# Optimization experiments

Measured on AMD Instinct MI355X. Metric: run time of the kernel, lower is better.

The kernel has to match this reference:

```python
import jax, jax.numpy as jnp
import numpy as np

D_MODEL = 768
N_HEADS = 12
D_K = D_MODEL // N_HEADS


def setup_inputs() -> dict:
    key = jax.random.key(0)
    ks = jax.random.split(key, 9)
    B, S = 4, 2048
    sc = 1.0 / np.sqrt(D_MODEL)
    inp = {"x": jax.random.normal(ks[0], (B, S, D_MODEL), dtype=jnp.float32)}
    names = ["q", "k", "v", "o"]
    for i, n in enumerate(names):
        inp[f"W{n}"] = jax.random.normal(ks[1 + 2 * i], (D_MODEL, D_MODEL), dtype=jnp.float32) * sc
        inp[f"b{n}"] = jax.random.normal(ks[2 + 2 * i], (D_MODEL,), dtype=jnp.float32) * 0.01
    return inp


def reference(x, Wq, bq, Wk, bk, Wv, bv, Wo, bo):
    B, S, _ = x.shape
    def split_heads(t):  # [B,S,D] -> [B,H,S,d_k]
        return t.reshape(B, S, N_HEADS, D_K).transpose(0, 2, 1, 3)
    Q = split_heads(x @ Wq.T + bq)
    K = split_heads(x @ Wk.T + bk)
    V = split_heads(x @ Wv.T + bv)
    # NOTE: original divides by d_k, not sqrt(d_k)
    scores = jnp.einsum("bhqd,bhkd->bhqk", Q, K) / D_K
    scores = jax.nn.softmax(scores, axis=-1)
    att = jnp.einsum("bhqk,bhkd->bhqd", scores, V)  # [B,H,S,d_k]
    att = att.transpose(0, 2, 1, 3).reshape(B, S, D_MODEL)
    return att @ Wo.T + bo
```

## Files before the change

### kernel.cpp

```cpp
#include <hip/hip_runtime.h>
#include <hip/hip_bf16.h>

typedef __bf16 bf16;
typedef _Float16 f16;
typedef bf16 bf16x8 __attribute__((ext_vector_type(8)));
typedef bf16 bf16x4 __attribute__((ext_vector_type(4)));
typedef f16 f16x4 __attribute__((ext_vector_type(4)));
typedef float f32x4 __attribute__((ext_vector_type(4)));

#define SLEN 2048
#define HEADS 12
#define DMODEL 768

#define GLOAD16(g, l) \
    __builtin_amdgcn_global_load_lds((const __attribute__((address_space(1))) void*)(g), \
                                     (__attribute__((address_space(3))) void*)(l), 16, 0, 0)

__global__ void cvt_kernel(const float* __restrict__ src, bf16* __restrict__ dst, int n4) {
    int idx = blockIdx.x * blockDim.x + threadIdx.x;
    if (idx < n4) {
        float4 v = ((const float4*)src)[idx];
        bf16x4 o;
        o[0] = (bf16)v.x; o[1] = (bf16)v.y; o[2] = (bf16)v.z; o[3] = (bf16)v.w;
        *(bf16x4*)(dst + (size_t)idx * 4) = o;
    }
}

__global__ void cvt4_kernel(const float* __restrict__ s0, const float* __restrict__ s1,
                            const float* __restrict__ s2, const float* __restrict__ s3,
                            bf16* __restrict__ d0, bf16* __restrict__ d1,
                            bf16* __restrict__ d2, bf16* __restrict__ d3, int n4) {
    const float* s; bf16* d;
    switch (blockIdx.y) {
        case 0: s = s0; d = d0; break;
        case 1: s = s1; d = d1; break;
        case 2: s = s2; d = d2; break;
        default: s = s3; d = d3; break;
    }
    int idx = blockIdx.x * blockDim.x + threadIdx.x;
    if (idx < n4) {
        float4 v = ((const float4*)s)[idx];
        bf16x4 o;
        o[0] = (bf16)v.x; o[1] = (bf16)v.y; o[2] = (bf16)v.z; o[3] = (bf16)v.w;
        *(bf16x4*)(d + (size_t)idx * 4) = o;
    }
}

__global__ __launch_bounds__(256, 3) void gemm_qkv(
    const bf16* __restrict__ A, const bf16* __restrict__ Bw,
    const float* __restrict__ bq, const float* __restrict__ bk, const float* __restrict__ bv,
    bf16* __restrict__ Qb, bf16* __restrict__ Kb, f16* __restrict__ VTb)
{
    __shared__ __align__(16) char smem[34048];
    typedef bf16 Tile[128][32];
    Tile* As = (Tile*)smem;
    Tile* Bs = (Tile*)(smem + 16384);
    const int K = DMODEL;
    int tid = threadIdx.x;
    int w = tid >> 6, lane = tid & 63, i16 = lane & 15, q4 = lane >> 4;
    int mblk = (w & 1) * 64, nblk = (w >> 1) * 64;
    int row0 = blockIdx.y * 128, col0 = blockIdx.x * 128;
    int srow = (lane >> 2), scol = (lane & 3) * 8;
    f32x4 acc[4][4] = {};

    const bf16* Ab = A  + (size_t)(row0 + w * 16 + srow) * K + scol;
    const bf16* Bb = Bw + (size_t)(col0 + w * 16 + srow) * K + scol;

#define STAGE(buf, k0) do { \
        GLOAD16(Ab + (k0),                  &As[buf][w * 16][0]); \
        GLOAD16(Ab + (size_t)64 * K + (k0), &As[buf][w * 16 + 64][0]); \
        GLOAD16(Bb + (k0),                  &Bs[buf][w * 16][0]); \
        GLOAD16(Bb + (size_t)64 * K + (k0), &Bs[buf][w * 16 + 64][0]); \
    } while (0)

    STAGE(0, 0);
    __syncthreads();
    int buf = 0;
    for (int k0 = 0; k0 < K; k0 += 32, buf ^= 1) {
        if (k0 + 32 < K) STAGE(buf ^ 1, k0 + 32);
        bf16x8 af[4], bfr[4];
#pragma unroll
        for (int t = 0; t < 4; ++t) af[t] = *(const bf16x8*)(&As[buf][mblk + t * 16 + i16][q4 * 8]);
#pragma unroll
        for (int t = 0; t < 4; ++t) bfr[t] = *(const bf16x8*)(&Bs[buf][nblk + t * 16 + i16][q4 * 8]);
#pragma unroll
        for (int ct = 0; ct < 4; ++ct)
#pragma unroll
            for (int st = 0; st < 4; ++st)
                acc[ct][st] = __builtin_amdgcn_mfma_f32_16x16x32_bf16(bfr[ct], af[st], acc[ct][st], 0, 0, 0);
        __syncthreads();
    }
#undef STAGE

    int region = col0 / DMODEL;
    int cbase = col0 - region * DMODEL + nblk;

    if (region < 2) {
        const float* bias = region ? bk : bq;
        bf16* dstb = region ? Kb : Qb;
        float scale = region ? 1.0f : 0.0225421217f;
#pragma unroll
        for (int ct = 0; ct < 4; ++ct) {
#pragma unroll
            for (int st = 0; st < 4; ++st) {
                int c0 = cbase + ct * 16 + q4 * 4;
                int h = c0 >> 6, d0 = c0 & 63;
                int sg = row0 + mblk + st * 16 + i16;
                int b = sg >> 11, s = sg & 2047;
                float4 bb = *(const float4*)(bias + c0);
                bf16x4 o;
                if (region == 0) {
                    o[0] = (bf16)((acc[ct][st][0] + bb.x) * scale);
                    o[1] = (bf16)((acc[ct][st][1] + bb.y) * scale);
                    o[2] = (bf16)((acc[ct][st][2] + bb.z) * scale);
                    o[3] = (bf16)((acc[ct][st][3] + bb.w) * scale);
                } else {
                    o[0] = (bf16)(acc[ct][st][0] + bb.x);
                    o[1] = (bf16)(acc[ct][st][1] + bb.y);
                    o[2] = (bf16)(acc[ct][st][2] + bb.z);
                    o[3] = (bf16)(acc[ct][st][3] + bb.w);
                }
                *(bf16x4*)(dstb + (((size_t)(b * HEADS + h)) * SLEN + s) * 64 + d0) = o;
            }
        }
    } else {
        __syncthreads();
        f16 (*Cs)[132] = (f16(*)[132])smem;
#pragma unroll
        for (int ct = 0; ct < 4; ++ct) {
#pragma unroll
            for (int st = 0; st < 4; ++st) {
                int cg = cbase + ct * 16 + q4 * 4;
                float4 bb = *(const float4*)(bv + cg);
                f16x4 vv;
                vv[0] = (f16)(acc[ct][st][0] + bb.x);
                vv[1] = (f16)(acc[ct][st][1] + bb.y);
                vv[2] = (f16)(acc[ct][st][2] + bb.z);
                vv[3] = (f16)(acc[ct][st][3] + bb.w);
                *(f16x4*)(&Cs[mblk + st * 16 + i16][nblk + ct * 16 + q4 * 4]) = vv;
            }
        }
        __syncthreads();
        int cl = lane * 2;
        int cg = cbase - nblk + cl;
        int h = cg >> 6, d = cg & 63;
        int s0 = w * 32;
        int b = row0 >> 11, sg = (row0 & 2047) + s0;
        f16* dst0 = VTb + ((size_t)(b * HEADS + h) * 64 + d) * SLEN + sg;
        f16* dst1 = dst0 + SLEN;
#pragma unroll
        for (int j = 0; j < 4; ++j) {
            unsigned v[8];
#pragma unroll
            for (int i = 0; i < 8; ++i) v[i] = *(const unsigned*)(&Cs[s0 + j * 8 + i][cl]);
            unsigned lo[4], hi[4];
#pragma unroll
            for (int i = 0; i < 4; ++i) {
                lo[i] = (v[2 * i] & 0xffffu) | (v[2 * i + 1] << 16);
                hi[i] = (v[2 * i] >> 16) | (v[2 * i + 1] & 0xffff0000u);
            }
            *(uint4*)(dst0 + j * 8) = *(uint4*)lo;
            *(uint4*)(dst1 + j * 8) = *(uint4*)hi;
        }
    }
}

__global__ __launch_bounds__(256, 3) void gemm_out(
    const bf16* __restrict__ A, const bf16* __restrict__ Bw,
    const float* __restrict__ bo, float* __restrict__ out)
{
    __shared__ bf16 As[2][128][32];
    __shared__ bf16 Bs[2][128][32];
    const int K = DMODEL;
    int tid = threadIdx.x;
    int w = tid >> 6, lane = tid & 63, i16 = lane & 15, q4 = lane >> 4;
    int mblk = (w & 1) * 64, nblk = (w >> 1) * 64;
    int row0 = blockIdx.y * 128, col0 = blockIdx.x * 128;
    int srow = (lane >> 2), scol = (lane & 3) * 8;
    f32x4 acc[4][4] = {};

    const bf16* Ab = A  + (size_t)(row0 + w * 16 + srow) * K + scol;
    const bf16* Bb = Bw + (size_t)(col0 + w * 16 + srow) * K + scol;

#define STAGE(buf, k0) do { \
        GLOAD16(Ab + (k0),                  &As[buf][w * 16][0]); \
        GLOAD16(Ab + (size_t)64 * K + (k0), &As[buf][w * 16 + 64][0]); \
        GLOAD16(Bb + (k0),                  &Bs[buf][w * 16][0]); \
        GLOAD16(Bb + (size_t)64 * K + (k0), &Bs[buf][w * 16 + 64][0]); \
    } while (0)

    STAGE(0, 0);
    __syncthreads();
    int buf = 0;
    for (int k0 = 0; k0 < K; k0 += 32, buf ^= 1) {
        if (k0 + 32 < K) STAGE(buf ^ 1, k0 + 32);
        bf16x8 af[4], bfr[4];
#pragma unroll
        for (int t = 0; t < 4; ++t) af[t] = *(const bf16x8*)(&As[buf][mblk + t * 16 + i16][q4 * 8]);
#pragma unroll
        for (int t = 0; t < 4; ++t) bfr[t] = *(const bf16x8*)(&Bs[buf][nblk + t * 16 + i16][q4 * 8]);
#pragma unroll
        for (int ct = 0; ct < 4; ++ct)
#pragma unroll
            for (int st = 0; st < 4; ++st)
                acc[ct][st] = __builtin_amdgcn_mfma_f32_16x16x32_bf16(bfr[ct], af[st], acc[ct][st], 0, 0, 0);
        __syncthreads();
    }
#undef STAGE

#pragma unroll
    for (int ct = 0; ct < 4; ++ct) {
#pragma unroll
        for (int st = 0; st < 4; ++st) {
            int c0 = col0 + nblk + ct * 16 + q4 * 4;
            int s = row0 + mblk + st * 16 + i16;
            float4 bb = *(const float4*)(bo + c0);
            float4 o = {acc[ct][st][0] + bb.x, acc[ct][st][1] + bb.y,
                        acc[ct][st][2] + bb.z, acc[ct][st][3] + bb.w};
            *(float4*)(out + (size_t)s * DMODEL + c0) = o;
        }
    }
}

__global__ __launch_bounds__(256, 4) void attn_kernel(
    const bf16* __restrict__ Qb, const bf16* __restrict__ Kb,
    const f16* __restrict__ VTb, bf16* __restrict__ att)
{
    __shared__ bf16 Ks[128][72];
    __shared__ f16  Vt[64][136];

    int tid = threadIdx.x;
    int w = tid >> 6, lane = tid & 63, i16 = lane & 15, q4 = lane >> 4;
    int qt = blockIdx.x, h = blockIdx.y, b = blockIdx.z;
    size_t bh = (size_t)b * HEADS + h;
    const bf16* Qp = Qb + (bh * SLEN + qt * 128 + w * 32) * 64;
    const bf16* Kp = Kb + bh * SLEN * 64;
    const f16*  Vp = VTb + bh * 64 * SLEN;

    bf16x8 aq[2][2];
#pragma unroll
    for (int qs = 0; qs < 2; ++qs) {
        aq[qs][0] = *(const bf16x8*)(Qp + (qs * 16 + i16) * 64 + q4 * 8);
        aq[qs][1] = *(const bf16x8*)(Qp + (qs * 16 + i16) * 64 + 32 + q4 * 8);
    }

    f32x4 oacc[2][4] = {};
    float lsum[2] = {0.f, 0.f};

    for (int kt = 0; kt < 16; ++kt) {
        int k0 = kt * 128;
        __syncthreads();
#pragma unroll
        for (int it = 0; it < 4; ++it) {
            int cidx = it * 256 + tid;
            int key = cidx >> 3, c8 = cidx & 7;
            *(uint4*)(&Ks[key][c8 * 8]) = *(const uint4*)(Kp + (size_t)(k0 + key) * 64 + c8 * 8);
            int d = cidx >> 4, c16 = cidx & 15;
            *(uint4*)(&Vt[d][c16 * 8]) = *(const uint4*)(Vp + (size_t)d * SLEN + k0 + c16 * 8);
        }
        __syncthreads();

        f16x4 pf[2][8];
#pragma unroll
        for (int t = 0; t < 8; ++t) {
            bf16x8 kf0 = *(const bf16x8*)(&Ks[t * 16 + i16][q4 * 8]);
            bf16x8 kf1 = *(const bf16x8*)(&Ks[t * 16 + i16][32 + q4 * 8]);
#pragma unroll
            for (int qs = 0; qs < 2; ++qs) {
                f32x4 z = {};
                z = __builtin_amdgcn_mfma_f32_16x16x32_bf16(kf0, aq[qs][0], z, 0, 0, 0);
                z = __builtin_amdgcn_mfma_f32_16x16x32_bf16(kf1, aq[qs][1], z, 0, 0, 0);
                f16x4 p;
#pragma unroll
                for (int r = 0; r < 4; ++r) {
                    float e = __builtin_amdgcn_exp2f(z[r]);
                    lsum[qs] += e;
                    p[r] = (f16)e;
                }
                pf[qs][t] = p;
            }
        }

#pragma unroll
        for (int t = 0; t < 8; ++t) {
#pragma unroll
            for (int dt = 0; dt < 4; ++dt) {
                f16x4 vf = *(const f16x4*)(&Vt[dt * 16 + i16][t * 16 + q4 * 4]);
                oacc[0][dt] = __builtin_amdgcn_mfma_f32_16x16x16f16(vf, pf[0][t], oacc[0][dt], 0, 0, 0);
                oacc[1][dt] = __builtin_amdgcn_mfma_f32_16x16x16f16(vf, pf[1][t], oacc[1][dt], 0, 0, 0);
            }
        }
    }

#pragma unroll
    for (int qs = 0; qs < 2; ++qs) {
        float l = lsum[qs];
        l += __shfl_xor(l, 16);
        l += __shfl_xor(l, 32);
        float inv = 1.f / l;
        int row = qt * 128 + w * 32 + qs * 16 + i16;
        size_t obase = ((size_t)b * SLEN + row) * DMODEL + h * 64;
#pragma unroll
        for (int dt = 0; dt < 4; ++dt) {
            bf16x4 o;
#pragma unroll
            for (int r = 0; r < 4; ++r) o[r] = (bf16)(oacc[qs][dt][r] * inv);
            *(bf16x4*)(att + obase + dt * 16 + q4 * 4) = o;
        }
    }
}

extern "C" void kernel_launch(void* const* d_in, const int* in_sizes, int n_in,
                              void* d_out, int out_size, void* d_ws, size_t ws_size,
                              hipStream_t stream) {
    const float* x  = (const float*)d_in[0];
    const float* Wq = (const float*)d_in[1];
    const float* bq = (const float*)d_in[2];
    const float* Wk = (const float*)d_in[3];
    const float* bk = (const float*)d_in[4];
    const float* Wv = (const float*)d_in[5];
    const float* bv = (const float*)d_in[6];
    const float* Wo = (const float*)d_in[7];
    const float* bo = (const float*)d_in[8];
    float* out = (float*)d_out;

    char* ws = (char*)d_ws;
    bf16* xb   = (bf16*)(ws);
    bf16* wqkv = (bf16*)(ws + 12582912);
    bf16* wob  = (bf16*)(ws + 16121856);
    bf16* Qb   = (bf16*)(ws + 17301504);
    bf16* Kb   = (bf16*)(ws + 29884416);
    f16*  VTb  = (f16*)(ws + 42467328);
    bf16* attb = xb;

    cvt_kernel<<<6144, 256, 0, stream>>>(x, xb, 1572864);
    cvt4_kernel<<<dim3(576, 4), 256, 0, stream>>>(Wq, Wk, Wv, Wo,
                                                  wqkv, wqkv + 589824, wqkv + 1179648, wob, 147456);

    gemm_qkv<<<dim3(18, 64), 256, 0, stream>>>(xb, wqkv, bq, bk, bv, Qb, Kb, VTb);
    attn_kernel<<<dim3(16, 12, 4), 256, 0, stream>>>(Qb, Kb, VTb, attb);
    gemm_out<<<dim3(6, 64), 256, 0, stream>>>(attb, wob, bo, out);
}
```

Before: 246.8 us.

## Enlarge QKV GEMM N-tile to 256 and attention Q-tile to 256 rows

The QKV projection GEMM now computes 128x256 tiles, so each block loads twice as much B data per A load and the grid is halved. The V-transpose epilogue is now done in two 128-column passes through shared memory. The attention kernel processes 64 query rows per wave (256 per block), reusing each K/V tile loaded into LDS across twice as many queries, and interleaves the QK and PV MFMAs per key subtile. The aim is to cut shared-memory and global traffic per FLOP, at the cost of higher register pressure, lower occupancy and fewer blocks (384 attention blocks, 576 GEMM blocks).

```diff
diff --git a/kernel.cpp b/kernel.cpp
--- a/kernel.cpp
+++ b/kernel.cpp
@@ -46,31 +46,34 @@
     }
 }
 
-__global__ __launch_bounds__(256, 3) void gemm_qkv(
+__global__ __launch_bounds__(256, 2) void gemm_qkv(
     const bf16* __restrict__ A, const bf16* __restrict__ Bw,
     const float* __restrict__ bq, const float* __restrict__ bk, const float* __restrict__ bv,
     bf16* __restrict__ Qb, bf16* __restrict__ Kb, f16* __restrict__ VTb)
 {
-    __shared__ __align__(16) char smem[34048];
-    typedef bf16 Tile[128][32];
-    Tile* As = (Tile*)smem;
-    Tile* Bs = (Tile*)(smem + 16384);
+    __shared__ __align__(16) char smem[49152];
+    typedef bf16 ATile[128][32];
+    typedef bf16 BTile[256][32];
+    ATile* As = (ATile*)smem;
+    BTile* Bs = (BTile*)(smem + 16384);
     const int K = DMODEL;
     int tid = threadIdx.x;
     int w = tid >> 6, lane = tid & 63, i16 = lane & 15, q4 = lane >> 4;
-    int mblk = (w & 1) * 64, nblk = (w >> 1) * 64;
-    int row0 = blockIdx.y * 128, col0 = blockIdx.x * 128;
-    int srow = (lane >> 2), scol = (lane & 3) * 8;
-    f32x4 acc[4][4] = {};
+    int mblk = (w & 1) * 64, nblk = (w >> 1) * 128;
+    int row0 = blockIdx.y * 128, col0 = blockIdx.x * 256;
+    int srow = lane >> 2, scol = (lane & 3) * 8;
+    f32x4 acc[8][4] = {};
 
     const bf16* Ab = A  + (size_t)(row0 + w * 16 + srow) * K + scol;
     const bf16* Bb = Bw + (size_t)(col0 + w * 16 + srow) * K + scol;
 
 #define STAGE(buf, k0) do { \
-        GLOAD16(Ab + (k0),                  &As[buf][w * 16][0]); \
-        GLOAD16(Ab + (size_t)64 * K + (k0), &As[buf][w * 16 + 64][0]); \
-        GLOAD16(Bb + (k0),                  &Bs[buf][w * 16][0]); \
-        GLOAD16(Bb + (size_t)64 * K + (k0), &Bs[buf][w * 16 + 64][0]); \
+        GLOAD16(Ab + (k0),                   &As[buf][w * 16][0]); \
+        GLOAD16(Ab + (size_t)64 * K + (k0),  &As[buf][w * 16 + 64][0]); \
+        GLOAD16(Bb + (k0),                   &Bs[buf][w * 16][0]); \
+        GLOAD16(Bb + (size_t)64 * K + (k0),  &Bs[buf][w * 16 + 64][0]); \
+        GLOAD16(Bb + (size_t)128 * K + (k0), &Bs[buf][w * 16 + 128][0]); \
+        GLOAD16(Bb + (size_t)192 * K + (k0), &Bs[buf][w * 16 + 192][0]); \
     } while (0)
 
     STAGE(0, 0);
@@ -78,13 +81,13 @@
     int buf = 0;
     for (int k0 = 0; k0 < K; k0 += 32, buf ^= 1) {
         if (k0 + 32 < K) STAGE(buf ^ 1, k0 + 32);
-        bf16x8 af[4], bfr[4];
-#pragma unroll
-        for (int t = 0; t < 4; ++t) af[t] = *(const bf16x8*)(&As[buf][mblk + t * 16 + i16][q4 * 8]);
-#pragma unroll
-        for (int t = 0; t < 4; ++t) bfr[t] = *(const bf16x8*)(&Bs[buf][nblk + t * 16 + i16][q4 * 8]);
-#pragma unroll
-        for (int ct = 0; ct < 4; ++ct)
+        bf16x8 af[4], bfr[8];
+#pragma unroll
+        for (int t = 0; t < 4; ++t) af[t]  = *(const bf16x8*)(&As[buf][mblk + t * 16 + i16][q4 * 8]);
+#pragma unroll
+        for (int t = 0; t < 8; ++t) bfr[t] = *(const bf16x8*)(&Bs[buf][nblk + t * 16 + i16][q4 * 8]);
+#pragma unroll
+        for (int ct = 0; ct < 8; ++ct)
 #pragma unroll
             for (int st = 0; st < 4; ++st)
                 acc[ct][st] = __builtin_amdgcn_mfma_f32_16x16x32_bf16(bfr[ct], af[st], acc[ct][st], 0, 0, 0);
@@ -98,9 +101,8 @@
     if (region < 2) {
         const float* bias = region ? bk : bq;
         bf16* dstb = region ? Kb : Qb;
-        float scale = region ? 1.0f : 0.0225421217f;
-#pragma unroll
-        for (int ct = 0; ct < 4; ++ct) {
+#pragma unroll
+        for (int ct = 0; ct < 8; ++ct) {
 #pragma unroll
             for (int st = 0; st < 4; ++st) {
                 int c0 = cbase + ct * 16 + q4 * 4;
@@ -110,10 +112,10 @@
                 float4 bb = *(const float4*)(bias + c0);
                 bf16x4 o;
                 if (region == 0) {
-                    o[0] = (bf16)((acc[ct][st][0] + bb.x) * scale);
-                    o[1] = (bf16)((acc[ct][st][1] + bb.y) * scale);
-                    o[2] = (bf16)((acc[ct][st][2] + bb.z) * scale);
-                    o[3] = (bf16)((acc[ct][st][3] + bb.w) * scale);
+                    o[0] = (bf16)((acc[ct][st][0] + bb.x) * 0.0225421217f);
+                    o[1] = (bf16)((acc[ct][st][1] + bb.y) * 0.0225421217f);
+                    o[2] = (bf16)((acc[ct][st][2] + bb.z) * 0.0225421217f);
+                    o[3] = (bf16)((acc[ct][st][3] + bb.w) * 0.0225421217f);
                 } else {
                     o[0] = (bf16)(acc[ct][st][0] + bb.x);
                     o[1] = (bf16)(acc[ct][st][1] + bb.y);
@@ -124,43 +126,48 @@
             }
         }
     } else {
-        __syncthreads();
         f16 (*Cs)[132] = (f16(*)[132])smem;
 #pragma unroll
-        for (int ct = 0; ct < 4; ++ct) {
-#pragma unroll
-            for (int st = 0; st < 4; ++st) {
-                int cg = cbase + ct * 16 + q4 * 4;
-                float4 bb = *(const float4*)(bv + cg);
-                f16x4 vv;
-                vv[0] = (f16)(acc[ct][st][0] + bb.x);
-                vv[1] = (f16)(acc[ct][st][1] + bb.y);
-                vv[2] = (f16)(acc[ct][st][2] + bb.z);
-                vv[3] = (f16)(acc[ct][st][3] + bb.w);
-                *(f16x4*)(&Cs[mblk + st * 16 + i16][nblk + ct * 16 + q4 * 4]) = vv;
-            }
-        }
-        __syncthreads();
-        int cl = lane * 2;
-        int cg = cbase - nblk + cl;
-        int h = cg >> 6, d = cg & 63;
-        int s0 = w * 32;
-        int b = row0 >> 11, sg = (row0 & 2047) + s0;
-        f16* dst0 = VTb + ((size_t)(b * HEADS + h) * 64 + d) * SLEN + sg;
-        f16* dst1 = dst0 + SLEN;
-#pragma unroll
-        for (int j = 0; j < 4; ++j) {
-            unsigned v[8];
-#pragma unroll
-            for (int i = 0; i < 8; ++i) v[i] = *(const unsigned*)(&Cs[s0 + j * 8 + i][cl]);
-            unsigned lo[4], hi[4];
-#pragma unroll
-            for (int i = 0; i < 4; ++i) {
-                lo[i] = (v[2 * i] & 0xffffu) | (v[2 * i + 1] << 16);
-                hi[i] = (v[2 * i] >> 16) | (v[2 * i + 1] & 0xffff0000u);
-            }
-            *(uint4*)(dst0 + j * 8) = *(uint4*)lo;
-            *(uint4*)(dst1 + j * 8) = *(uint4*)hi;
+        for (int p = 0; p < 2; ++p) {
+            if ((w >> 1) == p) {
+#pragma unroll
+                for (int ct = 0; ct < 8; ++ct) {
+#pragma unroll
+                    for (int st = 0; st < 4; ++st) {
+                        int cg = cbase + ct * 16 + q4 * 4;
+                        float4 bb = *(const float4*)(bv + cg);
+                        f16x4 vv;
+                        vv[0] = (f16)(acc[ct][st][0] + bb.x);
+                        vv[1] = (f16)(acc[ct][st][1] + bb.y);
+                        vv[2] = (f16)(acc[ct][st][2] + bb.z);
+                        vv[3] = (f16)(acc[ct][st][3] + bb.w);
+                        *(f16x4*)(&Cs[mblk + st * 16 + i16][ct * 16 + q4 * 4]) = vv;
+                    }
+                }
+            }
+            __syncthreads();
+            int cl = lane * 2;
+            int cg = (col0 - 2 * DMODEL) + p * 128 + cl;
+            int h = cg >> 6, d = cg & 63;
+            int s0 = w * 32;
+            int b = row0 >> 11, sg = (row0 & 2047) + s0;
+            f16* dst0 = VTb + ((size_t)(b * HEADS + h) * 64 + d) * SLEN + sg;
+            f16* dst1 = dst0 + SLEN;
+#pragma unroll
+            for (int j = 0; j < 4; ++j) {
+                unsigned v[8];
+#pragma unroll
+                for (int i = 0; i < 8; ++i) v[i] = *(const unsigned*)(&Cs[s0 + j * 8 + i][cl]);
+                unsigned lo[4], hi[4];
+#pragma unroll
+                for (int i = 0; i < 4; ++i) {
+                    lo[i] = (v[2 * i] & 0xffffu) | (v[2 * i + 1] << 16);
+                    hi[i] = (v[2 * i] >> 16) | (v[2 * i + 1] & 0xffff0000u);
+                }
+                *(uint4*)(dst0 + j * 8) = *(uint4*)lo;
+                *(uint4*)(dst1 + j * 8) = *(uint4*)hi;
+            }
+            __syncthreads();
         }
     }
 }
@@ -222,7 +229,7 @@
     }
 }
 
-__global__ __launch_bounds__(256, 4) void attn_kernel(
+__global__ __launch_bounds__(256, 2) void attn_kernel(
     const bf16* __restrict__ Qb, const bf16* __restrict__ Kb,
     const f16* __restrict__ VTb, bf16* __restrict__ att)
 {
@@ -233,19 +240,19 @@
     int w = tid >> 6, lane = tid & 63, i16 = lane & 15, q4 = lane >> 4;
     int qt = blockIdx.x, h = blockIdx.y, b = blockIdx.z;
     size_t bh = (size_t)b * HEADS + h;
-    const bf16* Qp = Qb + (bh * SLEN + qt * 128 + w * 32) * 64;
+    const bf16* Qp = Qb + (bh * SLEN + qt * 256 + w * 64) * 64;
     const bf16* Kp = Kb + bh * SLEN * 64;
     const f16*  Vp = VTb + bh * 64 * SLEN;
 
-    bf16x8 aq[2][2];
-#pragma unroll
-    for (int qs = 0; qs < 2; ++qs) {
+    bf16x8 aq[4][2];
+#pragma unroll
+    for (int qs = 0; qs < 4; ++qs) {
         aq[qs][0] = *(const bf16x8*)(Qp + (qs * 16 + i16) * 64 + q4 * 8);
         aq[qs][1] = *(const bf16x8*)(Qp + (qs * 16 + i16) * 64 + 32 + q4 * 8);
     }
 
-    f32x4 oacc[2][4] = {};
-    float lsum[2] = {0.f, 0.f};
+    f32x4 oacc[4][4] = {};
+    float lsum[4] = {0.f, 0.f, 0.f, 0.f};
 
     for (int kt = 0; kt < 16; ++kt) {
         int k0 = kt * 128;
@@ -260,45 +267,40 @@
         }
         __syncthreads();
 
-        f16x4 pf[2][8];
 #pragma unroll
         for (int t = 0; t < 8; ++t) {
             bf16x8 kf0 = *(const bf16x8*)(&Ks[t * 16 + i16][q4 * 8]);
             bf16x8 kf1 = *(const bf16x8*)(&Ks[t * 16 + i16][32 + q4 * 8]);
-#pragma unroll
-            for (int qs = 0; qs < 2; ++qs) {
+            f16x4 pf[4];
+#pragma unroll
+            for (int qs = 0; qs < 4; ++qs) {
                 f32x4 z = {};
                 z = __builtin_amdgcn_mfma_f32_16x16x32_bf16(kf0, aq[qs][0], z, 0, 0, 0);
                 z = __builtin_amdgcn_mfma_f32_16x16x32_bf16(kf1, aq[qs][1], z, 0, 0, 0);
-                f16x4 p;
 #pragma unroll
                 for (int r = 0; r < 4; ++r) {
                     float e = __builtin_amdgcn_exp2f(z[r]);
                     lsum[qs] += e;
-                    p[r] = (f16)e;
+                    pf[qs][r] = (f16)e;
                 }
-                pf[qs][t] = p;
-            }
-        }
-
-#pragma unroll
-        for (int t = 0; t < 8; ++t) {
+            }
 #pragma unroll
             for (int dt = 0; dt < 4; ++dt) {
                 f16x4 vf = *(const f16x4*)(&Vt[dt * 16 + i16][t * 16 + q4 * 4]);
-                oacc[0][dt] = __builtin_amdgcn_mfma_f32_16x16x16f16(vf, pf[0][t], oacc[0][dt], 0, 0, 0);
-                oacc[1][dt] = __builtin_amdgcn_mfma_f32_16x16x16f16(vf, pf[1][t], oacc[1][dt], 0, 0, 0);
-            }
-        }
-    }
-
-#pragma unroll
-    for (int qs = 0; qs < 2; ++qs) {
+#pragma unroll
+                for (int qs = 0; qs < 4; ++qs)
+                    oacc[qs][dt] = __builtin_amdgcn_mfma_f32_16x16x16f16(vf, pf[qs], oacc[qs][dt], 0, 0, 0);
+            }
+        }
+    }
+
+#pragma unroll
+    for (int qs = 0; qs < 4; ++qs) {
         float l = lsum[qs];
         l += __shfl_xor(l, 16);
         l += __shfl_xor(l, 32);
         float inv = 1.f / l;
-        int row = qt * 128 + w * 32 + qs * 16 + i16;
+        int row = qt * 256 + w * 64 + qs * 16 + i16;
         size_t obase = ((size_t)b * SLEN + row) * DMODEL + h * 64;
 #pragma unroll
         for (int dt = 0; dt < 4; ++dt) {
@@ -337,7 +339,7 @@
     cvt4_kernel<<<dim3(576, 4), 256, 0, stream>>>(Wq, Wk, Wv, Wo,
                                                   wqkv, wqkv + 589824, wqkv + 1179648, wob, 147456);
 
-    gemm_qkv<<<dim3(18, 64), 256, 0, stream>>>(xb, wqkv, bq, bk, bv, Qb, Kb, VTb);
-    attn_kernel<<<dim3(16, 12, 4), 256, 0, stream>>>(Qb, Kb, VTb, attb);
+    gemm_qkv<<<dim3(9, 64), 256, 0, stream>>>(xb, wqkv, bq, bk, bv, Qb, Kb, VTb);
+    attn_kernel<<<dim3(8, 12, 4), 256, 0, stream>>>(Qb, Kb, VTb, attb);
     gemm_out<<<dim3(6, 64), 256, 0, stream>>>(attb, wob, bo, out);
 }
```

Result: slower. 267.1 us (+8.2%).
